# Kernel optimization log

Hardware: AMD Instinct MI355X
Metric: run time of the kernel (lower is better)

## Reference

```python
import jax, jax.numpy as jnp
import numpy as np

D_IN = 1024
D_OUT = 1024
BATCH = 32
E = D_OUT + 2 * D_IN + 4  # 3076


def setup_inputs() -> dict:
    key = jax.random.key(0)
    k1, k2 = jax.random.split(key)
    x = jax.random.normal(k1, (BATCH, D_IN), dtype=jnp.float32)
    # xavier-ish scale for the fast-weight matrix
    w = jax.random.normal(k2, (BATCH, E, D_IN), dtype=jnp.float32) * 0.02
    return {"x": x, "w": w}


def reference(x, w):
    b = x.shape[0]
    # one batched matvec against the fast weights: [b,e,d] @ [b,d] -> [b,e]
    out = jnp.einsum('bed,bd->be', w, x)
    y = out[:, :D_OUT]
    k = out[:, D_OUT:D_OUT + D_IN]
    q = out[:, D_OUT + D_IN:D_OUT + 2 * D_IN]
    b1 = out[:, -4:-3]
    b2 = out[:, -3:-2]
    b3 = out[:, -2:-1]
    b4 = out[:, -1:]
    kphi = jax.nn.softmax(k, axis=1)
    qphi = jax.nn.softmax(q, axis=1)
    vbar = jnp.einsum('bed,bd->be', w, kphi)
    v = jnp.einsum('bed,bd->be', w, qphi)
    beta = jnp.concatenate([
        jnp.broadcast_to(b1, (b, D_OUT)),
        jnp.broadcast_to(b2, (b, D_IN)),
        jnp.broadcast_to(b3, (b, D_IN)),
        jnp.broadcast_to(b4, (b, 4)),
    ], axis=1)  # [b, e]
    # gated outer-product delta rule: dw = sigmoid(beta) * (v - vbar) kphi^T
    dw = jax.nn.sigmoid(beta)[:, :, None] * jnp.einsum('be,bd->bed', v - vbar, kphi)
    w_out = w + dw
    return (y, w_out)
```

## Files before the change

kernel.cpp:

```cpp
#include <hip/hip_runtime.h>
#include <cstddef>

constexpr int kDIn  = 1024;
constexpr int kDOut = 1024;
constexpr int kBatch = 32;
constexpr int kE = kDOut + 2 * kDIn + 4;
constexpr int kKQRows = 2 * kDIn + 4;
constexpr int kRowsKQ = kBatch * kKQRows;
constexpr int kRowsTotal = kBatch * kE;

typedef float floatx4 __attribute__((ext_vector_type(4)));

__device__ __forceinline__ float dot4(float4 a, float4 b) {
    return a.x * b.x + a.y * b.y + a.z * b.z + a.w * b.w;
}
__device__ __forceinline__ float dot4v(floatx4 a, float4 b) {
    return a.x * b.x + a.y * b.y + a.z * b.z + a.w * b.w;
}

__device__ __forceinline__ float dppSumTo63(float v) {
    int t;
    t = __builtin_amdgcn_update_dpp(0, __float_as_int(v), 0x111, 0xf, 0xf, true); v += __int_as_float(t);
    t = __builtin_amdgcn_update_dpp(0, __float_as_int(v), 0x112, 0xf, 0xf, true); v += __int_as_float(t);
    t = __builtin_amdgcn_update_dpp(0, __float_as_int(v), 0x114, 0xf, 0xf, true); v += __int_as_float(t);
    t = __builtin_amdgcn_update_dpp(0, __float_as_int(v), 0x118, 0xf, 0xf, true); v += __int_as_float(t);
    t = __builtin_amdgcn_update_dpp(0, __float_as_int(v), 0x142, 0xa, 0xf, true); v += __int_as_float(t);
    t = __builtin_amdgcn_update_dpp(0, __float_as_int(v), 0x143, 0xc, 0xf, true); v += __int_as_float(t);
    return v;
}

__device__ __forceinline__ float waveBcast63(float v) {
    return __int_as_float(__builtin_amdgcn_readlane(__float_as_int(v), 63));
}

__global__ __launch_bounds__(256) void k_matvec_kq(const float* __restrict__ w,
                                                   const float* __restrict__ x,
                                                   float* __restrict__ outv) {
    const int gw   = (blockIdx.x * 256 + threadIdx.x) >> 6;
    const int lane = threadIdx.x & 63;
    const int b = gw / kKQRows;
    const int e = kDOut + (gw % kKQRows);

    const float4* __restrict__ wr = (const float4*)(w + ((size_t)b * kE + e) * kDIn);
    const float4* __restrict__ xr = (const float4*)(x + (size_t)b * kDIn);

    float acc = 0.f;
#pragma unroll
    for (int it = 0; it < 4; ++it) {
        const int idx = it * 64 + lane;
        acc += dot4(wr[idx], xr[idx]);
    }
    acc = waveBcast63(dppSumTo63(acc));
    if (lane == 0) outv[(size_t)b * kE + e] = acc;
}

__global__ __launch_bounds__(256) void k_softmax_pair(const float* __restrict__ outv,
                                                      float* __restrict__ kphi,
                                                      float* __restrict__ dphi) {
    const int b   = blockIdx.x;
    const int tid = threadIdx.x;
    const float* __restrict__ base = outv + (size_t)b * kE + kDOut;

    const float4 kv = ((const float4*)base)[tid];
    const float4 qv = ((const float4*)(base + kDIn))[tid];

    float mk = fmaxf(fmaxf(kv.x, kv.y), fmaxf(kv.z, kv.w));
    float mq = fmaxf(fmaxf(qv.x, qv.y), fmaxf(qv.z, qv.w));
#pragma unroll
    for (int off = 32; off; off >>= 1) {
        mk = fmaxf(mk, __shfl_xor(mk, off, 64));
        mq = fmaxf(mq, __shfl_xor(mq, off, 64));
    }
    __shared__ float smk[4], smq[4];
    if ((tid & 63) == 0) { smk[tid >> 6] = mk; smq[tid >> 6] = mq; }
    __syncthreads();
    mk = fmaxf(fmaxf(smk[0], smk[1]), fmaxf(smk[2], smk[3]));
    mq = fmaxf(fmaxf(smq[0], smq[1]), fmaxf(smq[2], smq[3]));

    float4 ek, eq;
    ek.x = __expf(kv.x - mk); ek.y = __expf(kv.y - mk);
    ek.z = __expf(kv.z - mk); ek.w = __expf(kv.w - mk);
    eq.x = __expf(qv.x - mq); eq.y = __expf(qv.y - mq);
    eq.z = __expf(qv.z - mq); eq.w = __expf(qv.w - mq);
    float sk = ek.x + ek.y + ek.z + ek.w;
    float sq = eq.x + eq.y + eq.z + eq.w;
#pragma unroll
    for (int off = 32; off; off >>= 1) {
        sk += __shfl_xor(sk, off, 64);
        sq += __shfl_xor(sq, off, 64);
    }
    __shared__ float ssk[4], ssq[4];
    if ((tid & 63) == 0) { ssk[tid >> 6] = sk; ssq[tid >> 6] = sq; }
    __syncthreads();
    sk = ssk[0] + ssk[1] + ssk[2] + ssk[3];
    sq = ssq[0] + ssq[1] + ssq[2] + ssq[3];
    const float ik = 1.f / sk;
    const float iq = 1.f / sq;

    float4 kp, dp;
    kp.x = ek.x * ik; kp.y = ek.y * ik; kp.z = ek.z * ik; kp.w = ek.w * ik;
    dp.x = eq.x * iq - kp.x; dp.y = eq.y * iq - kp.y;
    dp.z = eq.z * iq - kp.z; dp.w = eq.w * iq - kp.w;
    ((float4*)(kphi + (size_t)b * kDIn))[tid] = kp;
    ((float4*)(dphi + (size_t)b * kDIn))[tid] = dp;
}

__global__ __launch_bounds__(256) void k_update(const float* __restrict__ w,
                                                const float* __restrict__ x,
                                                const float* __restrict__ outv,
                                                const float* __restrict__ kphi,
                                                const float* __restrict__ dphi,
                                                float* __restrict__ y_out,
                                                float* __restrict__ w_out) {
    const int gw   = (blockIdx.x * 256 + threadIdx.x) >> 6;
    const int lane = threadIdx.x & 63;

    int b, e;
    bool isY;
    if (gw < kRowsKQ) {
        const int idx = kRowsKQ - 1 - gw;
        b = idx / kKQRows;
        e = kDOut + (idx % kKQRows);
        isY = false;
    } else {
        const int gy = gw - kRowsKQ;
        b = gy >> 10;
        e = gy & 1023;
        isY = true;
    }

    const size_t row_off = ((size_t)b * kE + e) * kDIn;
    const float4*  __restrict__ wr  = (const float4*)(w + row_off);
    const floatx4* __restrict__ wrn = (const floatx4*)(w + row_off);
    const float4*  __restrict__ kr  = (const float4*)(kphi + (size_t)b * kDIn);
    const float4*  __restrict__ dr  = (const float4*)(dphi + (size_t)b * kDIn);

    floatx4 wv[4];
    float acc_d = 0.f, acc_y = 0.f;
    if (isY) {
        const float4* __restrict__ xr = (const float4*)(x + (size_t)b * kDIn);
#pragma unroll
        for (int it = 0; it < 4; ++it) {
            const int idx = it * 64 + lane;
            wv[it] = __builtin_nontemporal_load(&wrn[idx]);
            const float4 dv = dr[idx];
            const float4 xv = xr[idx];
            acc_d += dot4v(wv[it], dv);
            acc_y += dot4v(wv[it], xv);
        }
        acc_d = dppSumTo63(acc_d);
        acc_y = dppSumTo63(acc_y);
        acc_d = waveBcast63(acc_d);
        acc_y = waveBcast63(acc_y);
    } else {
#pragma unroll
        for (int it = 0; it < 4; ++it) {
            const int idx = it * 64 + lane;
            const float4 wl = wr[idx];
            wv[it].x = wl.x; wv[it].y = wl.y; wv[it].z = wl.z; wv[it].w = wl.w;
            const float4 dv = dr[idx];
            acc_d += dot4v(wv[it], dv);
        }
        acc_d = waveBcast63(dppSumTo63(acc_d));
    }

    const int bi = isY ? 0 : (e < kDOut + kDIn) ? 1 : (e < kDOut + 2 * kDIn) ? 2 : 3;
    const float beta = outv[(size_t)b * kE + (kE - 4) + bi];
    const float sig  = 1.f / (1.f + __expf(-beta));
    const float coef = sig * acc_d;

    floatx4* __restrict__ orow = (floatx4*)(w_out + row_off);
#pragma unroll
    for (int it = 0; it < 4; ++it) {
        const int idx = it * 64 + lane;
        const float4 kv = kr[idx];
        floatx4 o;
        o.x = wv[it].x + coef * kv.x;
        o.y = wv[it].y + coef * kv.y;
        o.z = wv[it].z + coef * kv.z;
        o.w = wv[it].w + coef * kv.w;
        __builtin_nontemporal_store(o, &orow[idx]);
    }

    if (isY && lane == 0) y_out[(size_t)b * kDOut + e] = acc_y;
}

extern "C" void kernel_launch(void* const* d_in, const int* in_sizes, int n_in,
                              void* d_out, int out_size, void* d_ws, size_t ws_size,
                              hipStream_t stream) {
    const float* x = (const float*)d_in[0];
    const float* w = (const float*)d_in[1];

    float* y_out = (float*)d_out;
    float* w_out = (float*)d_out + (size_t)kBatch * kDOut;

    float* outv = (float*)d_ws;
    float* kphi = outv + (size_t)kBatch * kE;
    float* dphi = kphi + (size_t)kBatch * kDIn;

    {
        const int blocks = kRowsKQ / 4;
        k_matvec_kq<<<blocks, 256, 0, stream>>>(w, x, outv);
    }
    k_softmax_pair<<<kBatch, 256, 0, stream>>>(outv, kphi, dphi);

    {
        const int blocks = kRowsTotal / 4;
        k_update<<<blocks, 256, 0, stream>>>(w, x, outv, kphi, dphi, y_out, w_out);
    }
}
```

Baseline: 681.0 us.

## Fuse three kernels into one cooperative persistent kernel with grid syncs

Replaces the three separate launches (k/q matvec, softmax, update) with one cooperative persistent kernel. Waves grid-stride over rows and two grid.sync barriers separate the phases, with a fallback to the old three launches if the cooperative launch fails. The aim is to remove launch gaps and inter-kernel drain. In exchange, the grid is capped by occupancy, the softmax phase runs on only 32 blocks while the rest wait, and two grid-wide barriers are added. It also drops one redundant readlane broadcast.

```diff
diff --git a/kernel.cpp b/kernel.cpp
--- a/kernel.cpp
+++ b/kernel.cpp
@@ -1,5 +1,8 @@
 #include <hip/hip_runtime.h>
+#include <hip/hip_cooperative_groups.h>
 #include <cstddef>
+
+namespace cg = cooperative_groups;
 
 constexpr int kDIn  = 1024;
 constexpr int kDOut = 1024;
@@ -28,39 +31,33 @@
     t = __builtin_amdgcn_update_dpp(0, __float_as_int(v), 0x143, 0xc, 0xf, true); v += __int_as_float(t);
     return v;
 }
-
 __device__ __forceinline__ float waveBcast63(float v) {
     return __int_as_float(__builtin_amdgcn_readlane(__float_as_int(v), 63));
 }
 
-__global__ __launch_bounds__(256) void k_matvec_kq(const float* __restrict__ w,
-                                                   const float* __restrict__ x,
-                                                   float* __restrict__ outv) {
-    const int gw   = (blockIdx.x * 256 + threadIdx.x) >> 6;
-    const int lane = threadIdx.x & 63;
+__device__ __forceinline__ void matvec_kq_row(int gw, int lane,
+                                              const float* __restrict__ w,
+                                              const float* __restrict__ x,
+                                              float* __restrict__ outv) {
     const int b = gw / kKQRows;
-    const int e = kDOut + (gw % kKQRows);
-
+    const int e = kDOut + (gw - b * kKQRows);
     const float4* __restrict__ wr = (const float4*)(w + ((size_t)b * kE + e) * kDIn);
     const float4* __restrict__ xr = (const float4*)(x + (size_t)b * kDIn);
-
     float acc = 0.f;
 #pragma unroll
     for (int it = 0; it < 4; ++it) {
         const int idx = it * 64 + lane;
         acc += dot4(wr[idx], xr[idx]);
     }
-    acc = waveBcast63(dppSumTo63(acc));
-    if (lane == 0) outv[(size_t)b * kE + e] = acc;
-}
-
-__global__ __launch_bounds__(256) void k_softmax_pair(const float* __restrict__ outv,
-                                                      float* __restrict__ kphi,
-                                                      float* __restrict__ dphi) {
-    const int b   = blockIdx.x;
-    const int tid = threadIdx.x;
+    acc = dppSumTo63(acc);
+    if (lane == 63) outv[(size_t)b * kE + e] = acc;
+}
+
+__device__ __forceinline__ void softmax_pair_body(int b, int tid,
+                                                  const float* __restrict__ outv,
+                                                  float* __restrict__ kphi,
+                                                  float* __restrict__ dphi) {
     const float* __restrict__ base = outv + (size_t)b * kE + kDOut;
-
     const float4 kv = ((const float4*)base)[tid];
     const float4 qv = ((const float4*)(base + kDIn))[tid];
 
@@ -105,22 +102,20 @@
     ((float4*)(dphi + (size_t)b * kDIn))[tid] = dp;
 }
 
-__global__ __launch_bounds__(256) void k_update(const float* __restrict__ w,
-                                                const float* __restrict__ x,
-                                                const float* __restrict__ outv,
-                                                const float* __restrict__ kphi,
-                                                const float* __restrict__ dphi,
-                                                float* __restrict__ y_out,
-                                                float* __restrict__ w_out) {
-    const int gw   = (blockIdx.x * 256 + threadIdx.x) >> 6;
-    const int lane = threadIdx.x & 63;
-
+__device__ __forceinline__ void update_row(int gw, int lane,
+                                           const float* __restrict__ w,
+                                           const float* __restrict__ x,
+                                           const float* __restrict__ outv,
+                                           const float* __restrict__ kphi,
+                                           const float* __restrict__ dphi,
+                                           float* __restrict__ y_out,
+                                           float* __restrict__ w_out) {
     int b, e;
     bool isY;
     if (gw < kRowsKQ) {
         const int idx = kRowsKQ - 1 - gw;
         b = idx / kKQRows;
-        e = kDOut + (idx % kKQRows);
+        e = kDOut + (idx - b * kKQRows);
         isY = false;
     } else {
         const int gy = gw - kRowsKQ;
@@ -150,8 +145,6 @@
         }
         acc_d = dppSumTo63(acc_d);
         acc_y = dppSumTo63(acc_y);
-        acc_d = waveBcast63(acc_d);
-        acc_y = waveBcast63(acc_y);
     } else {
 #pragma unroll
         for (int it = 0; it < 4; ++it) {
@@ -161,8 +154,9 @@
             const float4 dv = dr[idx];
             acc_d += dot4v(wv[it], dv);
         }
-        acc_d = waveBcast63(dppSumTo63(acc_d));
-    }
+        acc_d = dppSumTo63(acc_d);
+    }
+    acc_d = waveBcast63(acc_d);
 
     const int bi = isY ? 0 : (e < kDOut + kDIn) ? 1 : (e < kDOut + 2 * kDIn) ? 2 : 3;
     const float beta = outv[(size_t)b * kE + (kE - 4) + bi];
@@ -182,7 +176,61 @@
         __builtin_nontemporal_store(o, &orow[idx]);
     }
 
-    if (isY && lane == 0) y_out[(size_t)b * kDOut + e] = acc_y;
+    if (isY && lane == 63) y_out[(size_t)b * kDOut + e] = acc_y;
+}
+
+__global__ __launch_bounds__(256) void k_fused(const float* __restrict__ w,
+                                               const float* __restrict__ x,
+                                               float* __restrict__ outv,
+                                               float* __restrict__ kphi,
+                                               float* __restrict__ dphi,
+                                               float* __restrict__ y_out,
+                                               float* __restrict__ w_out) {
+    cg::grid_group grid = cg::this_grid();
+    const int tid    = threadIdx.x;
+    const int lane   = tid & 63;
+    const int wib    = tid >> 6;
+    const int nWaves = gridDim.x * 4;
+    const int wave0  = blockIdx.x * 4 + wib;
+
+    for (int gw = wave0; gw < kRowsKQ; gw += nWaves)
+        matvec_kq_row(gw, lane, w, x, outv);
+
+    grid.sync();
+
+    if (blockIdx.x < kBatch)
+        softmax_pair_body(blockIdx.x, tid, outv, kphi, dphi);
+
+    grid.sync();
+
+    for (int gw = wave0; gw < kRowsTotal; gw += nWaves)
+        update_row(gw, lane, w, x, outv, kphi, dphi, y_out, w_out);
+}
+
+__global__ __launch_bounds__(256) void k_matvec_kq(const float* __restrict__ w,
+                                                   const float* __restrict__ x,
+                                                   float* __restrict__ outv) {
+    const int gw   = (blockIdx.x * 256 + threadIdx.x) >> 6;
+    const int lane = threadIdx.x & 63;
+    matvec_kq_row(gw, lane, w, x, outv);
+}
+
+__global__ __launch_bounds__(256) void k_softmax_pair(const float* __restrict__ outv,
+                                                      float* __restrict__ kphi,
+                                                      float* __restrict__ dphi) {
+    softmax_pair_body(blockIdx.x, threadIdx.x, outv, kphi, dphi);
+}
+
+__global__ __launch_bounds__(256) void k_update(const float* __restrict__ w,
+                                                const float* __restrict__ x,
+                                                const float* __restrict__ outv,
+                                                const float* __restrict__ kphi,
+                                                const float* __restrict__ dphi,
+                                                float* __restrict__ y_out,
+                                                float* __restrict__ w_out) {
+    const int gw   = (blockIdx.x * 256 + threadIdx.x) >> 6;
+    const int lane = threadIdx.x & 63;
+    update_row(gw, lane, w, x, outv, kphi, dphi, y_out, w_out);
 }
 
 extern "C" void kernel_launch(void* const* d_in, const int* in_sizes, int n_in,
@@ -198,14 +246,32 @@
     float* kphi = outv + (size_t)kBatch * kE;
     float* dphi = kphi + (size_t)kBatch * kDIn;
 
-    {
-        const int blocks = kRowsKQ / 4;
-        k_matvec_kq<<<blocks, 256, 0, stream>>>(w, x, outv);
-    }
-    k_softmax_pair<<<kBatch, 256, 0, stream>>>(outv, kphi, dphi);
-
-    {
-        const int blocks = kRowsTotal / 4;
-        k_update<<<blocks, 256, 0, stream>>>(w, x, outv, kphi, dphi, y_out, w_out);
-    }
-}
+    static int s_gridBlocks = 0;
+    if (s_gridBlocks == 0) {
+        int perCU = 0, numCU = 0, dev = 0;
+        (void)hipGetDevice(&dev);
+        hipError_t e1 = hipOccupancyMaxActiveBlocksPerMultiprocessor(&perCU, k_fused, 256, 0);
+        hipError_t e2 = hipDeviceGetAttribute(&numCU, hipDeviceAttributeMultiprocessorCount, dev);
+        if (e1 != hipSuccess || e2 != hipSuccess || perCU <= 0 || numCU <= 0)
+            s_gridBlocks = -1;
+        else
+            s_gridBlocks = perCU * numCU;
+        if (s_gridBlocks > 0 && s_gridBlocks < kBatch) s_gridBlocks = -1;
+    }
+
+    bool coopOK = false;
+    if (s_gridBlocks > 0) {
+        void* args[] = {(void*)&w, (void*)&x, (void*)&outv, (void*)&kphi,
+                        (void*)&dphi, (void*)&y_out, (void*)&w_out};
+        hipError_t e = hipLaunchCooperativeKernel(k_fused, dim3(s_gridBlocks), dim3(256),
+                                                  args, 0, stream);
+        coopOK = (e == hipSuccess);
+        if (!coopOK) s_gridBlocks = -1;
+    }
+
+    if (!coopOK) {
+        k_matvec_kq<<<kRowsKQ / 4, 256, 0, stream>>>(w, x, outv);
+        k_softmax_pair<<<kBatch, 256, 0, stream>>>(outv, kphi, dphi);
+        k_update<<<kRowsTotal / 4, 256, 0, stream>>>(w, x, outv, kphi, dphi, y_out, w_out);
+    }
+}
```

New measurement: 938.2 us. +37.8%, slower.
